# Kernel tuning notes

Measured on AMD Instinct MI355X. Metric: run time of the kernel, lower is better.

The kernel has to match this reference:

```python
import jax, jax.numpy as jnp
import numpy as np

B, M, H = 8192, 512, 1024
CORRUPTION_LEN = int(0.6 * M)  # int(corruption_rate * input_dim)


def setup_inputs() -> dict:
    key = jax.random.key(0)
    ks = jax.random.split(key, 10)
    anchor = jax.random.normal(ks[0], (B, M), jnp.float32)
    random_sample = jax.random.normal(ks[1], (B, M), jnp.float32)
    # per-row random permutation -> exactly CORRUPTION_LEN corrupted features per row
    u = jax.random.uniform(ks[2], (B, M))
    ranks = jnp.argsort(jnp.argsort(u, axis=1), axis=1)  # rank of each column in a random permutation
    corruption_mask = ranks < CORRUPTION_LEN
    s_in = 1.0 / np.sqrt(M)
    s_h = 1.0 / np.sqrt(H)
    enc_w0 = jax.random.normal(ks[3], (M, H), jnp.float32) * s_in
    enc_b0 = jnp.full((H,), 0.01, jnp.float32)
    enc_w = jax.random.normal(ks[4], (3, H, H), jnp.float32) * s_h
    enc_b = jnp.full((3, H), 0.01, jnp.float32)
    head_w = jax.random.normal(ks[5], (2, H, H), jnp.float32) * s_h
    head_b = jnp.full((2, H), 0.01, jnp.float32)
    return {
        "anchor": anchor,
        "random_sample": random_sample,
        "corruption_mask": corruption_mask,
        "enc_w0": enc_w0,
        "enc_b0": enc_b0,
        "enc_w": enc_w,
        "enc_b": enc_b,
        "head_w": head_w,
        "head_b": head_b,
    }


def _mlp(x, w0, b0, ws, bs):
    # first dense + relu
    h = jax.nn.relu(x @ w0 + b0)
    # remaining dense + relu layers (small fixed count)
    for i in range(ws.shape[0]):
        h = jax.nn.relu(h @ ws[i] + bs[i])
    return h


def _embed(x, enc_w0, enc_b0, enc_w, enc_b, head_w, head_b):
    h = _mlp(x, enc_w0, enc_b0, enc_w, enc_b)          # encoder: 4 dense+relu
    h = jax.nn.relu(h @ head_w[0] + head_b[0])          # head: 2 dense+relu
    h = jax.nn.relu(h @ head_w[1] + head_b[1])
    return h


def reference(anchor, random_sample, corruption_mask, enc_w0, enc_b0, enc_w, enc_b, head_w, head_b):
    positive = jnp.where(corruption_mask, random_sample, anchor)
    emb_anchor = _embed(anchor, enc_w0, enc_b0, enc_w, enc_b, head_w, head_b)
    emb_positive = _embed(positive, enc_w0, enc_b0, enc_w, enc_b, head_w, head_b)
    return (emb_anchor, emb_positive)
```

## Files before the change

### kernel.cpp

```cpp
#include <hip/hip_runtime.h>
#include <hip/hip_bf16.h>
#include <stdint.h>


typedef __bf16 bf16x8 __attribute__((ext_vector_type(8)));
typedef float  f32x4  __attribute__((ext_vector_type(4)));
typedef unsigned short u16x8 __attribute__((ext_vector_type(8)));

__device__ __forceinline__ void gload_lds16(const void* g, void* l) {
  __builtin_amdgcn_global_load_lds(
      (const __attribute__((address_space(1))) uint32_t*)g,
      (__attribute__((address_space(3))) uint32_t*)l, 16, 0, 0);
}

__device__ __forceinline__ void fsplit(float v, uint16_t& ho, uint16_t& lo) {
  __bf16 hb = (__bf16)v;
  float  r  = v - (float)hb;
  __bf16 lb = (__bf16)r;
  ho = __builtin_bit_cast(uint16_t, hb);
  lo = __builtin_bit_cast(uint16_t, lb);
}

__global__ void detect_mask_kernel(const uint8_t* __restrict__ mask,
                                   int* __restrict__ flag) {
  if (threadIdx.x == 0 && blockIdx.x == 0) {
    uint32_t or_hi = 0;
    for (int i = 0; i < 256; ++i)
      or_hi |= ((const uint32_t*)mask)[i] & 0xFFFFFF00u;
    *flag = (or_hi != 0) ? 1 : 0;
  }
}

__global__ void pack_kernel(const float* __restrict__ anchor,
                            const float* __restrict__ rnd,
                            const uint8_t* __restrict__ mask,
                            const int* __restrict__ mask_is_bytes,
                            uint16_t* __restrict__ Xop) {
  int t = blockIdx.x * 256 + threadIdx.x;
  int row = t >> 6;
  int idx = t & 63;
  int g = idx >> 2, c = idx & 3;
  int kbase = idx * 8;
  const float4* ap = (const float4*)(anchor + (size_t)row * 512 + kbase);
  const float4* rp = (const float4*)(rnd + (size_t)row * 512 + kbase);
  float a[8], r[8];
  *(float4*)&a[0] = ap[0]; *(float4*)&a[4] = ap[1];
  *(float4*)&r[0] = rp[0]; *(float4*)&r[4] = rp[1];
  uint32_t mb;
  if (*mask_is_bytes) {
    const uint32_t* mp = (const uint32_t*)(mask + (size_t)row * 512 + kbase);
    uint32_t w0 = mp[0], w1 = mp[1];
    mb = 0;
#pragma unroll
    for (int j = 0; j < 4; ++j) {
      mb |= ((w0 >> (8 * j)) & 1u) << j;
      mb |= ((w1 >> (8 * j)) & 1u) << (4 + j);
    }
  } else {
    const int* mi = (const int*)mask + (size_t)row * 512 + kbase;
    int4 m0 = ((const int4*)mi)[0], m1 = ((const int4*)mi)[1];
    mb = (m0.x ? 1u : 0) | (m0.y ? 2u : 0) | (m0.z ? 4u : 0) | (m0.w ? 8u : 0) |
         (m1.x ? 16u : 0) | (m1.y ? 32u : 0) | (m1.z ? 64u : 0) | (m1.w ? 128u : 0);
  }
  u16x8 ah, al, ph, pl;
#pragma unroll
  for (int j = 0; j < 8; ++j) {
    uint16_t h, lo;
    fsplit(a[j], h, lo); ah[j] = h; al[j] = lo;
    float pv = ((mb >> j) & 1u) ? r[j] : a[j];
    fsplit(pv, h, lo); ph[j] = h; pl[j] = lo;
  }
  int s = row & 7;
  size_t base = ((size_t)row * 16 + g) * 64;
  *(u16x8*)(Xop + base + (size_t)((c ^ s)) * 8) = ah;
  *(u16x8*)(Xop + base + (size_t)(((c + 4) ^ s)) * 8) = al;
  size_t pbase = ((size_t)(row + 8192) * 16 + g) * 64;
  *(u16x8*)(Xop + pbase + (size_t)((c ^ s)) * 8) = ph;
  *(u16x8*)(Xop + pbase + (size_t)(((c + 4) ^ s)) * 8) = pl;
}

__global__ void wprep_kernel(const float* __restrict__ W,
                             uint16_t* __restrict__ Bop, int K) {
  __shared__ float tbuf[32][33];
  int g = blockIdx.x, n0 = blockIdx.y * 32;
  int tid = threadIdx.x;
#pragma unroll
  for (int i = 0; i < 4; ++i)
    tbuf[(tid >> 5) + i * 8][tid & 31] =
        W[((size_t)g * 32 + (tid >> 5) + i * 8) * 1024 + n0 + (tid & 31)];
  __syncthreads();
  if (tid < 128) {
    int nl = tid >> 2, c = tid & 3;
    int n = n0 + nl, s = n & 7;
    u16x8 hi, lo;
#pragma unroll
    for (int j = 0; j < 8; ++j) {
      uint16_t h, l2;
      fsplit(tbuf[c * 8 + j][nl], h, l2);
      hi[j] = h; lo[j] = l2;
    }
    size_t base = ((size_t)n * (K / 32) + g) * 64;
    *(u16x8*)(Bop + base + (size_t)((c ^ s)) * 8) = hi;
    *(u16x8*)(Bop + base + (size_t)(((c + 4) ^ s)) * 8) = lo;
  }
}

__device__ __forceinline__ void mfma_row(f32x4* accrow, bf16x8 aH, bf16x8 aL,
                                         const bf16x8* bh, const bf16x8* bl) {
#pragma unroll
  for (int n = 0; n < 4; ++n) {
    accrow[n] = __builtin_amdgcn_mfma_f32_16x16x32_bf16(aH, bh[n], accrow[n], 0, 0, 0);
    accrow[n] = __builtin_amdgcn_mfma_f32_16x16x32_bf16(aH, bl[n], accrow[n], 0, 0, 0);
    accrow[n] = __builtin_amdgcn_mfma_f32_16x16x32_bf16(aL, bh[n], accrow[n], 0, 0, 0);
  }
}

template <int K, bool LAST>
__global__ __launch_bounds__(512, 2) void gemm_kernel(
    const uint16_t* __restrict__ Aop, const uint16_t* __restrict__ Bop,
    const float* __restrict__ bias,
    uint16_t* __restrict__ Yop, float* __restrict__ Yf) {
  constexpr int KG = K / 32;
  __shared__ uint16_t sA[2][256 * 64];
  __shared__ uint16_t sB[2][256 * 64];

  int bid = blockIdx.x;
  int xcd = bid & 7, lid = bid >> 3;
  int tm = xcd * 8 + (lid >> 2), tn = lid & 3;
  const int brow = tm * 256, bcol = tn * 256;

  const int tid = threadIdx.x;
  const int l = tid & 63, w = tid >> 6;
  const int wr = w >> 2, wc = w & 3;
  const int l15 = l & 15, c16 = l >> 4;

  f32x4 acc[8][4];
#pragma unroll
  for (int m = 0; m < 8; ++m)
#pragma unroll
    for (int n = 0; n < 4; ++n) acc[m][n] = 0;

#define STAGE_A(g_, buf_)                                                     \
  _Pragma("unroll") for (int i = 0; i < 4; ++i) {                             \
    int row_ = i * 64 + (tid >> 3);                                           \
    gload_lds16(Aop + ((size_t)(brow + row_) * KG + (g_)) * 64 + (tid & 7) * 8,\
                &sA[buf_][i * 4096 + tid * 8]);                               \
  }
#define STAGE_B(g_, buf_)                                                     \
  _Pragma("unroll") for (int i = 0; i < 4; ++i) {                             \
    int row_ = i * 64 + (tid >> 3);                                           \
    gload_lds16(Bop + ((size_t)(bcol + row_) * KG + (g_)) * 64 + (tid & 7) * 8,\
                &sB[buf_][i * 4096 + tid * 8]);                               \
  }
#define READ_A(mm, aH, aL)                                                    \
  {                                                                           \
    int fr_ = wr * 128 + (mm)*16 + l15;                                       \
    const uint16_t* rp_ = pA + fr_ * 64;                                      \
    aH = *(const bf16x8*)(rp_ + ((c16 ^ (fr_ & 7))) * 8);                     \
    aL = *(const bf16x8*)(rp_ + (((c16 + 4) ^ (fr_ & 7))) * 8);               \
  }
#define BARRIER() __builtin_amdgcn_s_barrier()
#define LGKM0()                                                               \
  asm volatile("s_waitcnt lgkmcnt(0)" ::: "memory");                          \
  __builtin_amdgcn_sched_barrier(0)
#define VM0()                                                                 \
  asm volatile("s_waitcnt vmcnt(0)" ::: "memory");                            \
  __builtin_amdgcn_sched_barrier(0)

  STAGE_A(0, 0)
  STAGE_B(0, 0)
  VM0();
  BARRIER();

  int cur = 0;
#pragma unroll 1
  for (int g = 0; g < KG; ++g) {
    const uint16_t* pA = &sA[cur][0];
    const uint16_t* pB = &sB[cur][0];
    const bool pf = (g + 1 < KG);
    const int nxt = cur ^ 1;

    bf16x8 bh[4], bl[4];
#pragma unroll
    for (int n = 0; n < 4; ++n) {
      int fc = wc * 64 + n * 16 + l15;
      const uint16_t* rp = pB + fc * 64;
      bh[n] = *(const bf16x8*)(rp + ((c16 ^ (fc & 7))) * 8);
      bl[n] = *(const bf16x8*)(rp + (((c16 + 4) ^ (fc & 7))) * 8);
    }
    bf16x8 a0h, a0l, a1h, a1l;
    READ_A(0, a0h, a0l)
    READ_A(1, a1h, a1l)
    if (pf) { STAGE_A(g + 1, nxt) }
    BARRIER();
    LGKM0();
    __builtin_amdgcn_s_setprio(1);
    mfma_row(acc[0], a0h, a0l, bh, bl);
    mfma_row(acc[1], a1h, a1l, bh, bl);
    __builtin_amdgcn_s_setprio(0);
    BARRIER();

    bf16x8 a2h, a2l, a3h, a3l;
    READ_A(2, a2h, a2l)
    READ_A(3, a3h, a3l)
    if (pf) { STAGE_B(g + 1, nxt) }
    BARRIER();
    LGKM0();
    __builtin_amdgcn_s_setprio(1);
    mfma_row(acc[2], a2h, a2l, bh, bl);
    mfma_row(acc[3], a3h, a3l, bh, bl);
    __builtin_amdgcn_s_setprio(0);
    BARRIER();

    bf16x8 a4h, a4l, a5h, a5l;
    READ_A(4, a4h, a4l)
    READ_A(5, a5h, a5l)
    BARRIER();
    LGKM0();
    __builtin_amdgcn_s_setprio(1);
    mfma_row(acc[4], a4h, a4l, bh, bl);
    mfma_row(acc[5], a5h, a5l, bh, bl);
    __builtin_amdgcn_s_setprio(0);
    BARRIER();

    bf16x8 a6h, a6l, a7h, a7l;
    READ_A(6, a6h, a6l)
    READ_A(7, a7h, a7l)
    BARRIER();
    LGKM0();
    __builtin_amdgcn_s_setprio(1);
    mfma_row(acc[6], a6h, a6l, bh, bl);
    mfma_row(acc[7], a7h, a7l, bh, bl);
    __builtin_amdgcn_s_setprio(0);
    VM0();
    BARRIER();
    cur = nxt;
  }

  float bb[4];
  int colg[4], colc[4], cole[4];
#pragma unroll
  for (int n = 0; n < 4; ++n) {
    int col = bcol + wc * 64 + n * 16 + l15;
    bb[n] = bias[col];
    colg[n] = col >> 5; colc[n] = (col >> 3) & 3; cole[n] = col & 7;
  }
#pragma unroll
  for (int m = 0; m < 8; ++m) {
#pragma unroll
    for (int j = 0; j < 4; ++j) {
      int rowY = brow + wr * 128 + m * 16 + c16 * 4 + j;
      int s = rowY & 7;
#pragma unroll
      for (int n = 0; n < 4; ++n) {
        float v = acc[m][n][j] + bb[n];
        v = v > 0.f ? v : 0.f;
        if (LAST) {
          Yf[(size_t)rowY * 1024 + bcol + wc * 64 + n * 16 + l15] = v;
        } else {
          uint16_t h, lo2;
          fsplit(v, h, lo2);
          size_t base = ((size_t)rowY * 32 + colg[n]) * 64;
          Yop[base + (size_t)((colc[n] ^ s)) * 8 + cole[n]] = h;
          Yop[base + (size_t)(((colc[n] + 4) ^ s)) * 8 + cole[n]] = lo2;
        }
      }
    }
  }
#undef STAGE_A
#undef STAGE_B
#undef READ_A
#undef BARRIER
#undef LGKM0
#undef VM0
}

extern "C" void kernel_launch(void* const* d_in, const int* in_sizes, int n_in,
                              void* d_out, int out_size, void* d_ws, size_t ws_size,
                              hipStream_t stream) {
  (void)in_sizes; (void)n_in; (void)out_size; (void)ws_size;
  const float*   anchor = (const float*)d_in[0];
  const float*   rnd    = (const float*)d_in[1];
  const uint8_t* mask   = (const uint8_t*)d_in[2];
  const float*   enc_w0 = (const float*)d_in[3];
  const float*   enc_b0 = (const float*)d_in[4];
  const float*   enc_w  = (const float*)d_in[5];
  const float*   enc_b  = (const float*)d_in[6];
  const float*   head_w = (const float*)d_in[7];
  const float*   head_b = (const float*)d_in[8];
  float* out = (float*)d_out;

  const size_t WSZ0 = (size_t)512 * 2048;
  const size_t WSZ1 = (size_t)1024 * 2048;
  uint16_t* Wop = (uint16_t*)d_ws;
  size_t WOFF[6];
  WOFF[0] = 0;
  WOFF[1] = WSZ0;
  for (int i = 2; i < 6; ++i) WOFF[i] = WOFF[i - 1] + WSZ1;
  uint16_t* Xop = Wop + WOFF[5] + WSZ1;
  uint16_t* Yop = Xop + (size_t)16384 * 1024;
  int* mflag = (int*)(Yop + (size_t)16384 * 2048);
  uint16_t* Zop = (uint16_t*)d_out;

  detect_mask_kernel<<<1, 64, 0, stream>>>(mask, mflag);

  pack_kernel<<<2048, 256, 0, stream>>>(anchor, rnd, mask, mflag, Xop);

  wprep_kernel<<<dim3(16, 32), 256, 0, stream>>>(enc_w0, Wop + WOFF[0], 512);
  for (int i = 0; i < 3; ++i)
    wprep_kernel<<<dim3(32, 32), 256, 0, stream>>>(enc_w + (size_t)i * 1048576,
                                                   Wop + WOFF[1 + i], 1024);
  for (int i = 0; i < 2; ++i)
    wprep_kernel<<<dim3(32, 32), 256, 0, stream>>>(head_w + (size_t)i * 1048576,
                                                   Wop + WOFF[4 + i], 1024);

  dim3 g(256), b(512);
  gemm_kernel<512,  false><<<g, b, 0, stream>>>(Xop, Wop + WOFF[0], enc_b0,        Yop, nullptr);
  gemm_kernel<1024, false><<<g, b, 0, stream>>>(Yop, Wop + WOFF[1], enc_b,         Zop, nullptr);
  gemm_kernel<1024, false><<<g, b, 0, stream>>>(Zop, Wop + WOFF[2], enc_b + 1024,  Yop, nullptr);
  gemm_kernel<1024, false><<<g, b, 0, stream>>>(Yop, Wop + WOFF[3], enc_b + 2048,  Zop, nullptr);
  gemm_kernel<1024, false><<<g, b, 0, stream>>>(Zop, Wop + WOFF[4], head_b,        Yop, nullptr);
  gemm_kernel<1024, true ><<<g, b, 0, stream>>>(Yop, Wop + WOFF[5], head_b + 1024, nullptr, out);
}
```

Measured before the change: 586.0 us.

## Remove intra-iteration barriers and software-pipeline LDS reads against MFMAs

Drops the per-phase workgroup barriers and explicit lgkmcnt waits inside the K loop. LDS fragment reads for later rows are now issued while earlier MFMAs run, using two register sets. The A prefetch into the other buffer now starts at the top of the iteration. This is meant to cut barrier stalls and expose latency hiding to the compiler's own waitcnt insertion. It relies on the double buffer plus the end-of-iteration vmcnt wait and barrier for correctness, and reusing registers may add register pressure.

```diff
diff --git a/kernel.cpp b/kernel.cpp
--- a/kernel.cpp
+++ b/kernel.cpp
@@ -160,9 +160,6 @@
     aL = *(const bf16x8*)(rp_ + (((c16 + 4) ^ (fr_ & 7))) * 8);               \
   }
 #define BARRIER() __builtin_amdgcn_s_barrier()
-#define LGKM0()                                                               \
-  asm volatile("s_waitcnt lgkmcnt(0)" ::: "memory");                          \
-  __builtin_amdgcn_sched_barrier(0)
 #define VM0()                                                                 \
   asm volatile("s_waitcnt vmcnt(0)" ::: "memory");                            \
   __builtin_amdgcn_sched_barrier(0)
@@ -180,6 +177,8 @@
     const bool pf = (g + 1 < KG);
     const int nxt = cur ^ 1;
 
+    if (pf) { STAGE_A(g + 1, nxt) }
+
     bf16x8 bh[4], bl[4];
 #pragma unroll
     for (int n = 0; n < 4; ++n) {
@@ -188,50 +187,31 @@
       bh[n] = *(const bf16x8*)(rp + ((c16 ^ (fc & 7))) * 8);
       bl[n] = *(const bf16x8*)(rp + (((c16 + 4) ^ (fc & 7))) * 8);
     }
-    bf16x8 a0h, a0l, a1h, a1l;
+    bf16x8 a0h, a0l, a1h, a1l, a2h, a2l, a3h, a3l;
     READ_A(0, a0h, a0l)
     READ_A(1, a1h, a1l)
-    if (pf) { STAGE_A(g + 1, nxt) }
-    BARRIER();
-    LGKM0();
+    READ_A(2, a2h, a2l)
+    READ_A(3, a3h, a3l)
     __builtin_amdgcn_s_setprio(1);
     mfma_row(acc[0], a0h, a0l, bh, bl);
     mfma_row(acc[1], a1h, a1l, bh, bl);
     __builtin_amdgcn_s_setprio(0);
-    BARRIER();
-
-    bf16x8 a2h, a2l, a3h, a3l;
-    READ_A(2, a2h, a2l)
-    READ_A(3, a3h, a3l)
     if (pf) { STAGE_B(g + 1, nxt) }
-    BARRIER();
-    LGKM0();
+    READ_A(4, a0h, a0l)
+    READ_A(5, a1h, a1l)
     __builtin_amdgcn_s_setprio(1);
     mfma_row(acc[2], a2h, a2l, bh, bl);
     mfma_row(acc[3], a3h, a3l, bh, bl);
     __builtin_amdgcn_s_setprio(0);
-    BARRIER();
-
-    bf16x8 a4h, a4l, a5h, a5l;
-    READ_A(4, a4h, a4l)
-    READ_A(5, a5h, a5l)
-    BARRIER();
-    LGKM0();
+    READ_A(6, a2h, a2l)
+    READ_A(7, a3h, a3l)
     __builtin_amdgcn_s_setprio(1);
-    mfma_row(acc[4], a4h, a4l, bh, bl);
-    mfma_row(acc[5], a5h, a5l, bh, bl);
+    mfma_row(acc[4], a0h, a0l, bh, bl);
+    mfma_row(acc[5], a1h, a1l, bh, bl);
+    mfma_row(acc[6], a2h, a2l, bh, bl);
+    mfma_row(acc[7], a3h, a3l, bh, bl);
     __builtin_amdgcn_s_setprio(0);
-    BARRIER();
-
-    bf16x8 a6h, a6l, a7h, a7l;
-    READ_A(6, a6h, a6l)
-    READ_A(7, a7h, a7l)
-    BARRIER();
-    LGKM0();
-    __builtin_amdgcn_s_setprio(1);
-    mfma_row(acc[6], a6h, a6l, bh, bl);
-    mfma_row(acc[7], a7h, a7l, bh, bl);
-    __builtin_amdgcn_s_setprio(0);
+
     VM0();
     BARRIER();
     cur = nxt;
@@ -271,7 +251,6 @@
 #undef STAGE_B
 #undef READ_A
 #undef BARRIER
-#undef LGKM0
 #undef VM0
 }
 
```

After: 627.1 us. 1.07x slower.
